# Kernel optimization log

Hardware: AMD Instinct MI355X
Metric: run time of the kernel (lower is better)

Reference implementation:

```python
import jax, jax.numpy as jnp
from jax import lax
import numpy as np

B = 1048576       # batched program states
L = 64            # hidden width of LinearNNComplex
STEPS = 19        # While test: state[5] < var(19), step counter +1 per iter


def setup_inputs() -> dict:
    key = jax.random.key(0)
    ks = jax.random.split(key, 7)
    x = jax.random.normal(ks[0], (B, 6), dtype=jnp.float32)
    x = x.at[:, 5].set(0.0)  # step counter starts at 0 so the While runs 19 iters
    # LinearNNComplex params: Linear(2,L) -> ReLU -> Linear(L,L) -> ReLU -> Linear(L,3) -> Sigmoid
    s1 = 1.0 / np.sqrt(2.0)
    s2 = 1.0 / np.sqrt(float(L))
    W1 = jax.random.normal(ks[1], (2, L), dtype=jnp.float32) * s1
    b1 = jax.random.normal(ks[2], (L,), dtype=jnp.float32) * s1
    W2 = jax.random.normal(ks[3], (L, L), dtype=jnp.float32) * s2
    b2 = jax.random.normal(ks[4], (L,), dtype=jnp.float32) * s2
    W3 = jax.random.normal(ks[5], (L, 3), dtype=jnp.float32) * s2
    b3 = jax.random.normal(ks[6], (3,), dtype=jnp.float32) * s2
    return {"x": x, "W1": W1, "b1": b1, "W2": W2, "b2": b2, "W3": W3, "b3": b3}


def reference(x, W1, b1, W2, b2, W3, b3):
    """Batched Program interpreter.

    State columns: [0]=position, [1]=forward counter, [2:5]=branch probs,
    [5]=step counter. Each iteration:
      state[2:5] = sigmoid-MLP(state[0:2])            (assign_branch_probability)
      argmax over cols 2,3,4 picks branch:            (argmax_p)
        0 -> move_up    (col0 -= 1)
        1 -> move_right (col0 unchanged)
        2 -> move_down  (col0 += 1)
      state[1] += 1                                   (forward_update)
      state[5] += 1                                   (step_update)
    Runs STEPS=19 iterations (While: state[5] < 19).
    """
    def nn(z):  # z: [B, 2]
        h = jax.nn.relu(z @ W1 + b1)
        h = jax.nn.relu(h @ W2 + b2)
        return jax.nn.sigmoid(h @ W3 + b3)  # [B, 3]

    def body(state, _):
        p = nn(state[:, :2])                         # [B, 3]
        idx = jnp.argmax(p, axis=-1)                 # [B]
        delta = (idx - 1).astype(state.dtype)        # up=-1, right=0, down=+1
        new = jnp.concatenate(
            [
                (state[:, 0] + delta)[:, None],
                (state[:, 1] + 1.0)[:, None],
                p,
                (state[:, 5] + 1.0)[:, None],
            ],
            axis=-1,
        )
        return new, None

    final, _ = lax.scan(body, x, None, length=STEPS)
    return final  # [B, 6]
```

## Files before the change

### kernel.cpp

```cpp
#include <hip/hip_runtime.h>
#include <math.h>


#define NSTEPS 19

typedef _Float16 half8 __attribute__((ext_vector_type(8)));
typedef _Float16 half2v __attribute__((ext_vector_type(2)));
typedef float float4v __attribute__((ext_vector_type(4)));

__device__ __forceinline__ half2v pkrtz(float a, float b) {
    return __builtin_bit_cast(half2v, __builtin_amdgcn_cvt_pkrtz(a, b));
}

__device__ __forceinline__ float swz_xor16(float v) {
    int r = __builtin_amdgcn_ds_swizzle(__builtin_bit_cast(int, v), 0x401F);
    return __builtin_bit_cast(float, r);
}

__global__ __launch_bounds__(256, 2)
void program_kernel(const float* __restrict__ x,
                    const float* __restrict__ W1,
                    const float* __restrict__ b1,
                    const float* __restrict__ W2,
                    const float* __restrict__ b2,
                    const float* __restrict__ W3,
                    const float* __restrict__ b3,
                    float* __restrict__ out,
                    int B) {
    const int tid    = threadIdx.x;
    const int lane   = tid & 63;
    const int wave   = tid >> 6;
    const int lanelo = lane & 15;
    const int q8     = lane >> 4;
    const int rowBase = blockIdx.x * 64 + wave * 16;
    const int myRow   = rowBase + lanelo;
    const int rowLd   = myRow < B ? myRow : (B - 1);

    float w1a[16], w1b[16], b1v[16];
    #pragma unroll
    for (int j = 0; j < 8; ++j) {
        const int k0 = q8 * 8 + j;
        w1a[j]     = W1[k0];
        w1a[8 + j] = W1[32 + k0];
        w1b[j]     = W1[64 + k0];
        w1b[8 + j] = W1[96 + k0];
        b1v[j]     = b1[k0];
        b1v[8 + j] = b1[32 + k0];
    }

    half8 Wh[2][4], Wl[2][4];
    #pragma unroll
    for (int kf = 0; kf < 2; ++kf) {
        #pragma unroll
        for (int t = 0; t < 4; ++t) {
            half8 bh, bl;
            #pragma unroll
            for (int j = 0; j < 8; ++j) {
                const float w =
                    W2[(kf * 32 + q8 * 8 + j) * 64 + t * 16 + lanelo];
                const _Float16 wh = (_Float16)w;
                const _Float16 wl = (_Float16)((w - (float)wh) * 4096.0f);
                bh[j] = wh;
                bl[j] = wl;
            }
            Wh[kf][t] = bh;
            Wl[kf][t] = bl;
        }
    }

    float4v b2f[4];
    float w3v[4][4][3];
    #pragma unroll
    for (int t = 0; t < 4; ++t) {
        #pragma unroll
        for (int r = 0; r < 4; ++r) {
            const int n = t * 16 + q8 * 4 + r;
            b2f[t][r]    = b2[n];
            w3v[t][r][0] = W3[n * 3 + 0];
            w3v[t][r][1] = W3[n * 3 + 1];
            w3v[t][r][2] = W3[n * 3 + 2];
        }
    }
    const float b3v0 = b3[0], b3v1 = b3[1], b3v2 = b3[2];

    float pos, fwd, c5;
    {
        const float* xr = x + (size_t)rowLd * 6;
        pos = xr[0];
        fwd = xr[1];
        c5  = xr[5];
    }

    const float4v zf = {0.f, 0.f, 0.f, 0.f};
    float l0 = 0.f, l1 = 0.f, l2 = 0.f;

    #pragma unroll 1
    for (int step = 0; step < NSTEPS; ++step) {
        half8 Hh[2], Hl[2];
        #pragma unroll
        for (int kf = 0; kf < 2; ++kf) {
            float h[8];
            #pragma unroll
            for (int j = 0; j < 8; ++j) {
                const int e = kf * 8 + j;
                h[j] = fmaxf(0.f,
                             fmaf(pos, w1a[e], fmaf(fwd, w1b[e], b1v[e])));
            }
            union { half8 v; half2v p[4]; } uh, ul;
            #pragma unroll
            for (int p = 0; p < 4; ++p)
                uh.p[p] = pkrtz(h[2 * p], h[2 * p + 1]);
            #pragma unroll
            for (int p = 0; p < 4; ++p) {
                const float r0 =
                    (h[2 * p]     - (float)uh.p[p][0]) * 4096.0f;
                const float r1 =
                    (h[2 * p + 1] - (float)uh.p[p][1]) * 4096.0f;
                ul.p[p] = pkrtz(r0, r1);
            }
            Hh[kf] = uh.v;
            Hl[kf] = ul.v;
        }

        float4v accA[4], accB[4];
        #pragma unroll
        for (int t = 0; t < 4; ++t) {
            accB[t] = __builtin_amdgcn_mfma_f32_16x16x32_f16(
                Wl[0][t], Hh[0], zf, 0, 0, 0);
            accB[t] = __builtin_amdgcn_mfma_f32_16x16x32_f16(
                Wh[0][t], Hl[0], accB[t], 0, 0, 0);
            accB[t] = __builtin_amdgcn_mfma_f32_16x16x32_f16(
                Wl[1][t], Hh[1], accB[t], 0, 0, 0);
            accB[t] = __builtin_amdgcn_mfma_f32_16x16x32_f16(
                Wh[1][t], Hl[1], accB[t], 0, 0, 0);
            accA[t] = __builtin_amdgcn_mfma_f32_16x16x32_f16(
                Wh[0][t], Hh[0], b2f[t], 0, 0, 0);
            accA[t] = __builtin_amdgcn_mfma_f32_16x16x32_f16(
                Wh[1][t], Hh[1], accA[t], 0, 0, 0);
        }

        float s0 = 0.f, s1 = 0.f, s2 = 0.f;
        #pragma unroll
        for (int t = 0; t < 4; ++t) {
            #pragma unroll
            for (int r = 0; r < 4; ++r) {
                float h2 = fmaf(accB[t][r], 1.0f / 4096.0f, accA[t][r]);
                h2 = fmaxf(h2, 0.f);
                s0 = fmaf(h2, w3v[t][r][0], s0);
                s1 = fmaf(h2, w3v[t][r][1], s1);
                s2 = fmaf(h2, w3v[t][r][2], s2);
            }
        }
        s0 += swz_xor16(s0);
        s1 += swz_xor16(s1);
        s2 += swz_xor16(s2);
        s0 += __shfl_xor(s0, 32, 64);
        s1 += __shfl_xor(s1, 32, 64);
        s2 += __shfl_xor(s2, 32, 64);
        l0 = s0 + b3v0;
        l1 = s1 + b3v1;
        l2 = s2 + b3v2;

        const float m01   = fmaxf(l0, l1);
        const float delta = (l2 > m01) ? 1.0f : ((l1 > l0) ? 0.0f : -1.0f);
        pos += delta;
        fwd += 1.0f;
    }

    if (q8 == 0 && myRow < B) {
        const float p0 = 1.f / (1.f + __expf(-l0));
        const float p1 = 1.f / (1.f + __expf(-l1));
        const float p2 = 1.f / (1.f + __expf(-l2));
        float2* o = (float2*)(out + (size_t)myRow * 6);
        o[0] = make_float2(pos, fwd);
        o[1] = make_float2(p0, p1);
        o[2] = make_float2(p2, c5 + (float)NSTEPS);
    }
}

extern "C" void kernel_launch(void* const* d_in, const int* in_sizes, int n_in,
                              void* d_out, int out_size, void* d_ws, size_t ws_size,
                              hipStream_t stream) {
    const float* x  = (const float*)d_in[0];
    const float* W1 = (const float*)d_in[1];
    const float* b1 = (const float*)d_in[2];
    const float* W2 = (const float*)d_in[3];
    const float* b2 = (const float*)d_in[4];
    const float* W3 = (const float*)d_in[5];
    const float* b3 = (const float*)d_in[6];
    float* out = (float*)d_out;

    const int B = in_sizes[0] / 6;
    const int nBlocks = (B + 63) / 64;

    program_kernel<<<nBlocks, 256, 0, stream>>>(
        x, W1, b1, W2, b2, W3, b3, out, B);
}
```

Measured before the change: 686.2 us.

## Process two row tiles per wave and move W1/W3 tables to LDS

Each wave now handles 32 rows, as two 16-row MFMA tiles, instead of 16. This halves the number of blocks and amortizes the per-block W2 fp16 split setup over twice the rows. The W1/b1 and W3 per-lane register arrays move into shared-memory float4 tables, read each step, to free registers for the doubled accumulators. The cost is extra LDS reads in the inner loop and higher register pressure, which could reduce occupancy under launch_bounds(256,2). The second tile's independent MFMA chain can also hide latency.

```diff
diff --git a/kernel.cpp b/kernel.cpp
--- a/kernel.cpp
+++ b/kernel.cpp
@@ -4,9 +4,9 @@
 
 #define NSTEPS 19
 
-typedef _Float16 half8 __attribute__((ext_vector_type(8)));
+typedef _Float16 half8  __attribute__((ext_vector_type(8)));
 typedef _Float16 half2v __attribute__((ext_vector_type(2)));
-typedef float float4v __attribute__((ext_vector_type(4)));
+typedef float    float4v __attribute__((ext_vector_type(4)));
 
 __device__ __forceinline__ half2v pkrtz(float a, float b) {
     return __builtin_bit_cast(half2v, __builtin_amdgcn_cvt_pkrtz(a, b));
@@ -32,21 +32,30 @@
     const int wave   = tid >> 6;
     const int lanelo = lane & 15;
     const int q8     = lane >> 4;
-    const int rowBase = blockIdx.x * 64 + wave * 16;
-    const int myRow   = rowBase + lanelo;
-    const int rowLd   = myRow < B ? myRow : (B - 1);
-
-    float w1a[16], w1b[16], b1v[16];
-    #pragma unroll
-    for (int j = 0; j < 8; ++j) {
-        const int k0 = q8 * 8 + j;
-        w1a[j]     = W1[k0];
-        w1a[8 + j] = W1[32 + k0];
-        w1b[j]     = W1[64 + k0];
-        w1b[8 + j] = W1[96 + k0];
-        b1v[j]     = b1[k0];
-        b1v[8 + j] = b1[32 + k0];
-    }
+
+    __shared__ float4v w1t[12][4];
+    __shared__ float4v w3t[12][4];
+    for (int idx = tid; idx < 96; idx += 256) {
+        if (idx < 48) {
+            const int table = idx >> 4;
+            const int rem   = idx & 15;
+            const int q = rem >> 2, c = rem & 3;
+            const int k0 = q * 8 + (c & 1) * 4 + (c >> 1) * 32;
+            const float* src = (table == 0) ? (W1 + k0)
+                             : (table == 1) ? (W1 + 64 + k0)
+                                            : (b1 + k0);
+            w1t[table * 4 + c][q] = (float4v){src[0], src[1], src[2], src[3]};
+        } else {
+            const int j = idx - 48;
+            const int t = j / 12, rem = j % 12;
+            const int cc = rem >> 2, q = rem & 3;
+            const int n0 = 16 * t + 4 * q;
+            w3t[t * 3 + cc][q] =
+                (float4v){W3[(n0 + 0) * 3 + cc], W3[(n0 + 1) * 3 + cc],
+                          W3[(n0 + 2) * 3 + cc], W3[(n0 + 3) * 3 + cc]};
+        }
+    }
+    __syncthreads();
 
     half8 Wh[2][4], Wl[2][4];
     #pragma unroll
@@ -69,112 +78,146 @@
     }
 
     float4v b2f[4];
-    float w3v[4][4][3];
     #pragma unroll
     for (int t = 0; t < 4; ++t) {
-        #pragma unroll
-        for (int r = 0; r < 4; ++r) {
-            const int n = t * 16 + q8 * 4 + r;
-            b2f[t][r]    = b2[n];
-            w3v[t][r][0] = W3[n * 3 + 0];
-            w3v[t][r][1] = W3[n * 3 + 1];
-            w3v[t][r][2] = W3[n * 3 + 2];
-        }
+        const int n = t * 16 + q8 * 4;
+        b2f[t] = (float4v){b2[n], b2[n + 1], b2[n + 2], b2[n + 3]};
     }
     const float b3v0 = b3[0], b3v1 = b3[1], b3v2 = b3[2];
 
-    float pos, fwd, c5;
+    const int rowBase = blockIdx.x * 128 + wave * 32;
+    const int row0 = rowBase + lanelo;
+    const int row1 = rowBase + 16 + lanelo;
+    const int ld0 = row0 < B ? row0 : (B - 1);
+    const int ld1 = row1 < B ? row1 : (B - 1);
+
+    float pos[2], fwd[2], c5[2], l0[2], l1[2], l2[2];
     {
-        const float* xr = x + (size_t)rowLd * 6;
-        pos = xr[0];
-        fwd = xr[1];
-        c5  = xr[5];
-    }
+        const float* r = x + (size_t)ld0 * 6;
+        pos[0] = r[0]; fwd[0] = r[1]; c5[0] = r[5];
+        const float* s = x + (size_t)ld1 * 6;
+        pos[1] = s[0]; fwd[1] = s[1]; c5[1] = s[5];
+    }
+    l0[0] = l0[1] = l1[0] = l1[1] = l2[0] = l2[1] = 0.f;
 
     const float4v zf = {0.f, 0.f, 0.f, 0.f};
-    float l0 = 0.f, l1 = 0.f, l2 = 0.f;
 
     #pragma unroll 1
     for (int step = 0; step < NSTEPS; ++step) {
-        half8 Hh[2], Hl[2];
+        half8 Hh[2][2], Hl[2][2];
         #pragma unroll
         for (int kf = 0; kf < 2; ++kf) {
-            float h[8];
-            #pragma unroll
-            for (int j = 0; j < 8; ++j) {
-                const int e = kf * 8 + j;
-                h[j] = fmaxf(0.f,
-                             fmaf(pos, w1a[e], fmaf(fwd, w1b[e], b1v[e])));
-            }
-            union { half8 v; half2v p[4]; } uh, ul;
-            #pragma unroll
-            for (int p = 0; p < 4; ++p)
-                uh.p[p] = pkrtz(h[2 * p], h[2 * p + 1]);
-            #pragma unroll
-            for (int p = 0; p < 4; ++p) {
-                const float r0 =
-                    (h[2 * p]     - (float)uh.p[p][0]) * 4096.0f;
-                const float r1 =
-                    (h[2 * p + 1] - (float)uh.p[p][1]) * 4096.0f;
-                ul.p[p] = pkrtz(r0, r1);
-            }
-            Hh[kf] = uh.v;
-            Hl[kf] = ul.v;
-        }
-
-        float4v accA[4], accB[4];
-        #pragma unroll
-        for (int t = 0; t < 4; ++t) {
-            accB[t] = __builtin_amdgcn_mfma_f32_16x16x32_f16(
-                Wl[0][t], Hh[0], zf, 0, 0, 0);
-            accB[t] = __builtin_amdgcn_mfma_f32_16x16x32_f16(
-                Wh[0][t], Hl[0], accB[t], 0, 0, 0);
-            accB[t] = __builtin_amdgcn_mfma_f32_16x16x32_f16(
-                Wl[1][t], Hh[1], accB[t], 0, 0, 0);
-            accB[t] = __builtin_amdgcn_mfma_f32_16x16x32_f16(
-                Wh[1][t], Hl[1], accB[t], 0, 0, 0);
-            accA[t] = __builtin_amdgcn_mfma_f32_16x16x32_f16(
-                Wh[0][t], Hh[0], b2f[t], 0, 0, 0);
-            accA[t] = __builtin_amdgcn_mfma_f32_16x16x32_f16(
-                Wh[1][t], Hh[1], accA[t], 0, 0, 0);
-        }
-
-        float s0 = 0.f, s1 = 0.f, s2 = 0.f;
-        #pragma unroll
-        for (int t = 0; t < 4; ++t) {
-            #pragma unroll
-            for (int r = 0; r < 4; ++r) {
-                float h2 = fmaf(accB[t][r], 1.0f / 4096.0f, accA[t][r]);
-                h2 = fmaxf(h2, 0.f);
-                s0 = fmaf(h2, w3v[t][r][0], s0);
-                s1 = fmaf(h2, w3v[t][r][1], s1);
-                s2 = fmaf(h2, w3v[t][r][2], s2);
-            }
-        }
-        s0 += swz_xor16(s0);
-        s1 += swz_xor16(s1);
-        s2 += swz_xor16(s2);
-        s0 += __shfl_xor(s0, 32, 64);
-        s1 += __shfl_xor(s1, 32, 64);
-        s2 += __shfl_xor(s2, 32, 64);
-        l0 = s0 + b3v0;
-        l1 = s1 + b3v1;
-        l2 = s2 + b3v2;
-
-        const float m01   = fmaxf(l0, l1);
-        const float delta = (l2 > m01) ? 1.0f : ((l1 > l0) ? 0.0f : -1.0f);
-        pos += delta;
-        fwd += 1.0f;
-    }
-
-    if (q8 == 0 && myRow < B) {
-        const float p0 = 1.f / (1.f + __expf(-l0));
-        const float p1 = 1.f / (1.f + __expf(-l1));
-        const float p2 = 1.f / (1.f + __expf(-l2));
-        float2* o = (float2*)(out + (size_t)myRow * 6);
-        o[0] = make_float2(pos, fwd);
-        o[1] = make_float2(p0, p1);
-        o[2] = make_float2(p2, c5 + (float)NSTEPS);
+            float4v wa0 = w1t[kf * 2 + 0][q8], wa1 = w1t[kf * 2 + 1][q8];
+            float4v wb0 = w1t[4 + kf * 2 + 0][q8], wb1 = w1t[4 + kf * 2 + 1][q8];
+            float4v bb0 = w1t[8 + kf * 2 + 0][q8], bb1 = w1t[8 + kf * 2 + 1][q8];
+            #pragma unroll
+            for (int u = 0; u < 2; ++u) {
+                float h[8];
+                #pragma unroll
+                for (int i = 0; i < 4; ++i) {
+                    h[i] = fmaxf(0.f,
+                        fmaf(pos[u], wa0[i], fmaf(fwd[u], wb0[i], bb0[i])));
+                    h[4 + i] = fmaxf(0.f,
+                        fmaf(pos[u], wa1[i], fmaf(fwd[u], wb1[i], bb1[i])));
+                }
+                union { half8 v; half2v p[4]; } uh, ul;
+                #pragma unroll
+                for (int p = 0; p < 4; ++p)
+                    uh.p[p] = pkrtz(h[2 * p], h[2 * p + 1]);
+                #pragma unroll
+                for (int p = 0; p < 4; ++p) {
+                    const float r0 = (h[2 * p]     - (float)uh.p[p][0]) * 4096.0f;
+                    const float r1 = (h[2 * p + 1] - (float)uh.p[p][1]) * 4096.0f;
+                    ul.p[p] = pkrtz(r0, r1);
+                }
+                Hh[u][kf] = uh.v;
+                Hl[u][kf] = ul.v;
+            }
+        }
+
+        float4v accA[2][4], accB[2][4];
+        #pragma unroll
+        for (int u = 0; u < 2; ++u) {
+            #pragma unroll
+            for (int t = 0; t < 4; ++t) {
+                accB[u][t] = __builtin_amdgcn_mfma_f32_16x16x32_f16(
+                    Wl[0][t], Hh[u][0], zf, 0, 0, 0);
+                accB[u][t] = __builtin_amdgcn_mfma_f32_16x16x32_f16(
+                    Wh[0][t], Hl[u][0], accB[u][t], 0, 0, 0);
+                accB[u][t] = __builtin_amdgcn_mfma_f32_16x16x32_f16(
+                    Wl[1][t], Hh[u][1], accB[u][t], 0, 0, 0);
+                accB[u][t] = __builtin_amdgcn_mfma_f32_16x16x32_f16(
+                    Wh[1][t], Hl[u][1], accB[u][t], 0, 0, 0);
+                accA[u][t] = __builtin_amdgcn_mfma_f32_16x16x32_f16(
+                    Wh[0][t], Hh[u][0], b2f[t], 0, 0, 0);
+                accA[u][t] = __builtin_amdgcn_mfma_f32_16x16x32_f16(
+                    Wh[1][t], Hh[u][1], accA[u][t], 0, 0, 0);
+            }
+        }
+
+        #pragma unroll
+        for (int u = 0; u < 2; ++u) {
+            float4v h2[4];
+            #pragma unroll
+            for (int t = 0; t < 4; ++t) {
+                #pragma unroll
+                for (int r = 0; r < 4; ++r) {
+                    float v = fmaf(accB[u][t][r], 1.0f / 4096.0f, accA[u][t][r]);
+                    h2[t][r] = fmaxf(v, 0.f);
+                }
+            }
+            float s[3];
+            #pragma unroll
+            for (int c = 0; c < 3; ++c) {
+                float d[4];
+                #pragma unroll
+                for (int t = 0; t < 4; ++t) {
+                    const float4v w = w3t[t * 3 + c][q8];
+                    float a = h2[t][0] * w[0];
+                    a = fmaf(h2[t][1], w[1], a);
+                    a = fmaf(h2[t][2], w[2], a);
+                    a = fmaf(h2[t][3], w[3], a);
+                    d[t] = a;
+                }
+                s[c] = (d[0] + d[1]) + (d[2] + d[3]);
+            }
+            s[0] += swz_xor16(s[0]);
+            s[1] += swz_xor16(s[1]);
+            s[2] += swz_xor16(s[2]);
+            s[0] += __shfl_xor(s[0], 32, 64);
+            s[1] += __shfl_xor(s[1], 32, 64);
+            s[2] += __shfl_xor(s[2], 32, 64);
+            l0[u] = s[0] + b3v0;
+            l1[u] = s[1] + b3v1;
+            l2[u] = s[2] + b3v2;
+
+            const float m01 = fmaxf(l0[u], l1[u]);
+            const float delta =
+                (l2[u] > m01) ? 1.0f : ((l1[u] > l0[u]) ? 0.0f : -1.0f);
+            pos[u] += delta;
+            fwd[u] += 1.0f;
+        }
+    }
+
+    if (q8 == 0) {
+        if (row0 < B) {
+            const float p0 = 1.f / (1.f + __expf(-l0[0]));
+            const float p1 = 1.f / (1.f + __expf(-l1[0]));
+            const float p2 = 1.f / (1.f + __expf(-l2[0]));
+            float2* o = (float2*)(out + (size_t)row0 * 6);
+            o[0] = make_float2(pos[0], fwd[0]);
+            o[1] = make_float2(p0, p1);
+            o[2] = make_float2(p2, c5[0] + (float)NSTEPS);
+        }
+        if (row1 < B) {
+            const float p0 = 1.f / (1.f + __expf(-l0[1]));
+            const float p1 = 1.f / (1.f + __expf(-l1[1]));
+            const float p2 = 1.f / (1.f + __expf(-l2[1]));
+            float2* o = (float2*)(out + (size_t)row1 * 6);
+            o[0] = make_float2(pos[1], fwd[1]);
+            o[1] = make_float2(p0, p1);
+            o[2] = make_float2(p2, c5[1] + (float)NSTEPS);
+        }
     }
 }
 
@@ -191,7 +234,7 @@
     float* out = (float*)d_out;
 
     const int B = in_sizes[0] / 6;
-    const int nBlocks = (B + 63) / 64;
+    const int nBlocks = (B + 127) / 128;
 
     program_kernel<<<nBlocks, 256, 0, stream>>>(
         x, W1, b1, W2, b2, W3, b3, out, B);
```

New measurement: 659.3 us. -3.9%, faster.

## Use logit differences for argmax and packed float2 math in MLP epilogue

Applied to the files above, without the earlier changes.

The argmax now works on the differences of logits 1 and 2 from logit 0 (precomputed W3 and b3 column differences), which cuts the per-step output layer from three reductions to two. The full logit 0 is only computed on the last step, where it is needed for the sigmoid outputs. Layer-1 and epilogue arithmetic is rewritten with float2 elementwise FMA/max so the compiler can emit packed FP32 instructions. Computing differences first can change rounding slightly, which may flip argmax ties in rare cases.

```diff
diff --git a/kernel.cpp b/kernel.cpp
--- a/kernel.cpp
+++ b/kernel.cpp
@@ -4,17 +4,23 @@
 
 #define NSTEPS 19
 
-typedef _Float16 half8 __attribute__((ext_vector_type(8)));
-typedef _Float16 half2v __attribute__((ext_vector_type(2)));
-typedef float float4v __attribute__((ext_vector_type(4)));
+typedef _Float16 half8   __attribute__((ext_vector_type(8)));
+typedef _Float16 half2v  __attribute__((ext_vector_type(2)));
+typedef float    float2v __attribute__((ext_vector_type(2)));
+typedef float    float4v __attribute__((ext_vector_type(4)));
 
 __device__ __forceinline__ half2v pkrtz(float a, float b) {
     return __builtin_bit_cast(half2v, __builtin_amdgcn_cvt_pkrtz(a, b));
 }
-
 __device__ __forceinline__ float swz_xor16(float v) {
     int r = __builtin_amdgcn_ds_swizzle(__builtin_bit_cast(int, v), 0x401F);
     return __builtin_bit_cast(float, r);
+}
+__device__ __forceinline__ float2v lo2(float4v v) {
+    return __builtin_shufflevector(v, v, 0, 1);
+}
+__device__ __forceinline__ float2v hi2(float4v v) {
+    return __builtin_shufflevector(v, v, 2, 3);
 }
 
 __global__ __launch_bounds__(256, 2)
@@ -32,20 +38,22 @@
     const int wave   = tid >> 6;
     const int lanelo = lane & 15;
     const int q8     = lane >> 4;
-    const int rowBase = blockIdx.x * 64 + wave * 16;
-    const int myRow   = rowBase + lanelo;
-    const int rowLd   = myRow < B ? myRow : (B - 1);
-
-    float w1a[16], w1b[16], b1v[16];
-    #pragma unroll
-    for (int j = 0; j < 8; ++j) {
-        const int k0 = q8 * 8 + j;
-        w1a[j]     = W1[k0];
-        w1a[8 + j] = W1[32 + k0];
-        w1b[j]     = W1[64 + k0];
-        w1b[8 + j] = W1[96 + k0];
-        b1v[j]     = b1[k0];
-        b1v[8 + j] = b1[32 + k0];
+    const int myRow  = blockIdx.x * 64 + wave * 16 + lanelo;
+    const int rowLd  = myRow < B ? myRow : (B - 1);
+
+    float2v w1a[8], w1b[8], b1v[8];
+    #pragma unroll
+    for (int kf = 0; kf < 2; ++kf) {
+        const int k0 = kf * 32 + q8 * 8;
+        const float2v* a = (const float2v*)(W1 + k0);
+        const float2v* bb = (const float2v*)(W1 + 64 + k0);
+        const float2v* bv = (const float2v*)(b1 + k0);
+        #pragma unroll
+        for (int i = 0; i < 4; ++i) {
+            w1a[kf * 4 + i] = a[i];
+            w1b[kf * 4 + i] = bb[i];
+            b1v[kf * 4 + i] = bv[i];
+        }
     }
 
     half8 Wh[2][4], Wl[2][4];
@@ -69,19 +77,26 @@
     }
 
     float4v b2f[4];
-    float w3v[4][4][3];
     #pragma unroll
     for (int t = 0; t < 4; ++t) {
-        #pragma unroll
-        for (int r = 0; r < 4; ++r) {
-            const int n = t * 16 + q8 * 4 + r;
-            b2f[t][r]    = b2[n];
-            w3v[t][r][0] = W3[n * 3 + 0];
-            w3v[t][r][1] = W3[n * 3 + 1];
-            w3v[t][r][2] = W3[n * 3 + 2];
-        }
-    }
-    const float b3v0 = b3[0], b3v1 = b3[1], b3v2 = b3[2];
+        const int n = t * 16 + q8 * 4;
+        b2f[t] = (float4v){b2[n], b2[n + 1], b2[n + 2], b2[n + 3]};
+    }
+
+    float2v d10[8], d20[8];
+    #pragma unroll
+    for (int p = 0; p < 8; ++p) {
+        const int n0 = (p >> 1) * 16 + q8 * 4 + (p & 1) * 2;
+        const float w00 = W3[n0 * 3 + 0],       w01 = W3[n0 * 3 + 1];
+        const float w02 = W3[n0 * 3 + 2];
+        const float w10 = W3[(n0 + 1) * 3 + 0], w11 = W3[(n0 + 1) * 3 + 1];
+        const float w12 = W3[(n0 + 1) * 3 + 2];
+        d10[p] = (float2v){w01 - w00, w11 - w10};
+        d20[p] = (float2v){w02 - w00, w12 - w10};
+    }
+    const float b3v0 = b3[0];
+    const float db10 = b3[1] - b3[0];
+    const float db20 = b3[2] - b3[0];
 
     float pos, fwd, c5;
     {
@@ -92,31 +107,28 @@
     }
 
     const float4v zf = {0.f, 0.f, 0.f, 0.f};
+    const float2v z2 = {0.f, 0.f};
+    const float2v kinv = {1.0f / 4096.0f, 1.0f / 4096.0f};
     float l0 = 0.f, l1 = 0.f, l2 = 0.f;
 
     #pragma unroll 1
     for (int step = 0; step < NSTEPS; ++step) {
+        const float2v posp = {pos, pos}, fwdp = {fwd, fwd};
         half8 Hh[2], Hl[2];
         #pragma unroll
         for (int kf = 0; kf < 2; ++kf) {
-            float h[8];
-            #pragma unroll
-            for (int j = 0; j < 8; ++j) {
-                const int e = kf * 8 + j;
-                h[j] = fmaxf(0.f,
-                             fmaf(pos, w1a[e], fmaf(fwd, w1b[e], b1v[e])));
-            }
-            union { half8 v; half2v p[4]; } uh, ul;
-            #pragma unroll
-            for (int p = 0; p < 4; ++p)
-                uh.p[p] = pkrtz(h[2 * p], h[2 * p + 1]);
+            union { half8 v; half2v h2[4]; } uh, ul;
             #pragma unroll
             for (int p = 0; p < 4; ++p) {
-                const float r0 =
-                    (h[2 * p]     - (float)uh.p[p][0]) * 4096.0f;
-                const float r1 =
-                    (h[2 * p + 1] - (float)uh.p[p][1]) * 4096.0f;
-                ul.p[p] = pkrtz(r0, r1);
+                const int e = kf * 4 + p;
+                float2v z = __builtin_elementwise_fma(fwdp, w1b[e], b1v[e]);
+                z = __builtin_elementwise_fma(posp, w1a[e], z);
+                const float2v hp = __builtin_elementwise_max(z, z2);
+                uh.h2[p] = pkrtz(hp[0], hp[1]);
+                const float r0 = fmaf((float)uh.h2[p][0], -1.0f, hp[0]);
+                const float r1 = fmaf((float)uh.h2[p][1], -1.0f, hp[1]);
+                const float2v rp = (float2v){r0, r1} * 4096.0f;
+                ul.h2[p] = pkrtz(rp[0], rp[1]);
             }
             Hh[kf] = uh.v;
             Hl[kf] = ul.v;
@@ -139,30 +151,50 @@
                 Wh[1][t], Hh[1], accA[t], 0, 0, 0);
         }
 
-        float s0 = 0.f, s1 = 0.f, s2 = 0.f;
+        float2v h2p[8];
         #pragma unroll
         for (int t = 0; t < 4; ++t) {
+            h2p[2 * t] = __builtin_elementwise_max(
+                __builtin_elementwise_fma(lo2(accB[t]), kinv, lo2(accA[t])),
+                z2);
+            h2p[2 * t + 1] = __builtin_elementwise_max(
+                __builtin_elementwise_fma(hi2(accB[t]), kinv, hi2(accA[t])),
+                z2);
+        }
+
+        float2v s1 = z2, s2 = z2;
+        #pragma unroll
+        for (int p = 0; p < 8; ++p) {
+            s1 = __builtin_elementwise_fma(h2p[p], d10[p], s1);
+            s2 = __builtin_elementwise_fma(h2p[p], d20[p], s2);
+        }
+        float g10 = s1[0] + s1[1];
+        float g20 = s2[0] + s2[1];
+        g10 += swz_xor16(g10);
+        g20 += swz_xor16(g20);
+        g10 += __shfl_xor(g10, 32, 64);
+        g20 += __shfl_xor(g20, 32, 64);
+        g10 += db10;
+        g20 += db20;
+
+        if (step == NSTEPS - 1) {
+            float2v s0 = z2;
             #pragma unroll
-            for (int r = 0; r < 4; ++r) {
-                float h2 = fmaf(accB[t][r], 1.0f / 4096.0f, accA[t][r]);
-                h2 = fmaxf(h2, 0.f);
-                s0 = fmaf(h2, w3v[t][r][0], s0);
-                s1 = fmaf(h2, w3v[t][r][1], s1);
-                s2 = fmaf(h2, w3v[t][r][2], s2);
+            for (int p = 0; p < 8; ++p) {
+                const int n0 = (p >> 1) * 16 + q8 * 4 + (p & 1) * 2;
+                const float2v w30 = {W3[n0 * 3], W3[(n0 + 1) * 3]};
+                s0 = __builtin_elementwise_fma(h2p[p], w30, s0);
             }
-        }
-        s0 += swz_xor16(s0);
-        s1 += swz_xor16(s1);
-        s2 += swz_xor16(s2);
-        s0 += __shfl_xor(s0, 32, 64);
-        s1 += __shfl_xor(s1, 32, 64);
-        s2 += __shfl_xor(s2, 32, 64);
-        l0 = s0 + b3v0;
-        l1 = s1 + b3v1;
-        l2 = s2 + b3v2;
-
-        const float m01   = fmaxf(l0, l1);
-        const float delta = (l2 > m01) ? 1.0f : ((l1 > l0) ? 0.0f : -1.0f);
+            float t0 = s0[0] + s0[1];
+            t0 += swz_xor16(t0);
+            t0 += __shfl_xor(t0, 32, 64);
+            l0 = t0 + b3v0;
+            l1 = l0 + g10;
+            l2 = l0 + g20;
+        }
+
+        const float delta =
+            (g20 > fmaxf(0.f, g10)) ? 1.0f : ((g10 > 0.f) ? 0.0f : -1.0f);
         pos += delta;
         fwd += 1.0f;
     }
```

Result: faster. 637.1 us (-7.2%).
